# Optimization experiments

Measured on AMD Instinct MI355X. Metric: run time of the kernel, lower is better.

Reference implementation:

```python
import jax, jax.numpy as jnp
import numpy as np

N_NODES = 100000
N_EDGES = 1600000
DIM_IN, DIM_HID, DIM_OUT = 256, 128, 64


def _gcn_norm(edge_index, num_nodes):
    # PyG gcn_norm with add_self_loops=True, symmetric normalization.
    loop = jnp.arange(num_nodes, dtype=edge_index.dtype)
    row = jnp.concatenate([edge_index[0], loop])  # source
    col = jnp.concatenate([edge_index[1], loop])  # destination
    deg = jax.ops.segment_sum(jnp.ones_like(col, dtype=jnp.float32), col,
                              num_segments=num_nodes)
    dis = jnp.where(deg > 0, jax.lax.rsqrt(deg), 0.0)
    norm = dis[row] * dis[col]  # [E + N]
    return row, col, norm


def _gcn_conv(x, row, col, norm, W, b, num_nodes):
    h = x @ W                      # [N, d_out] linear first (d_out <= d_in typical)
    msg = h[row] * norm[:, None]   # gather + edge scaling, [E+N, d_out]
    out = jax.ops.segment_sum(msg, col, num_segments=num_nodes)  # scatter-add
    return out + b


def setup_inputs() -> dict:
    key = jax.random.key(0)
    k1, k2, k3, k4, k5 = jax.random.split(key, 5)
    x = jax.random.normal(k1, (N_NODES, DIM_IN), dtype=jnp.float32)
    edge_index = jax.random.randint(k2, (2, N_EDGES), 0, N_NODES, dtype=jnp.int32)
    s1 = 1.0 / np.sqrt(DIM_IN)
    s2 = 1.0 / np.sqrt(DIM_HID)
    W1 = jax.random.uniform(k3, (DIM_IN, DIM_HID), jnp.float32, -s1, s1)
    b1 = jnp.zeros((DIM_HID,), jnp.float32)
    W2 = jax.random.uniform(k4, (DIM_HID, DIM_OUT), jnp.float32, -s2, s2)
    b2 = jnp.zeros((DIM_OUT,), jnp.float32)
    return {"x": x, "edge_index": edge_index, "W1": W1, "b1": b1,
            "W2": W2, "b2": b2}


def reference(x, edge_index, W1, b1, W2, b2):
    n = x.shape[0]
    row, col, norm = _gcn_norm(edge_index, n)  # cached=True: shared by both layers
    h = _gcn_conv(x, row, col, norm, W1, b1, n)
    h = jax.nn.relu(h)
    h = _gcn_conv(h, row, col, norm, W2, b2, n)
    return jax.nn.log_softmax(h, axis=-1)
```

## Files before the change

### kernel.cpp

```cpp
#include <hip/hip_runtime.h>

#define N_NODES 100000
#define N_EDGES 1600000
#define DIN 256
#define DHID 128
#define DOUT 64

#define BSHIFT 9
#define NBUCKET 196
#define CHUNK 4096
#define NCHUNK ((N_EDGES + CHUNK - 1) / CHUNK)

typedef __attribute__((ext_vector_type(8))) short bf16x8;
typedef __attribute__((ext_vector_type(4))) float f32x4;
typedef __attribute__((ext_vector_type(2))) float f32x2;

static __device__ __forceinline__ ushort f2bf(float f) {
  union { float f; uint u; } a; a.f = f;
  uint u = a.u;
  uint r = u + 0x7fffu + ((u >> 16) & 1u);
  return (ushort)(r >> 16);
}


#if __has_builtin(__builtin_amdgcn_cvt_pk_f32_fp8) && __has_builtin(__builtin_amdgcn_cvt_pk_fp8_f32) && __has_builtin(__builtin_amdgcn_cvt_f32_fp8)
#define FP8_HW 1
#else
#define FP8_HW 0
#endif

static __device__ __forceinline__ uint f2fp8(float f) {
#if FP8_HW
  return (uint)(__builtin_amdgcn_cvt_pk_fp8_f32(f, f, 0, false) & 0xFF);
#else
  uint u = __float_as_uint(f);
  uint s = (u >> 24) & 0x80u;
  u &= 0x7FFFFFFFu;
  u += 0x7FFFFu + ((u >> 20) & 1u);
  int e = (int)(u >> 23) - 120;
  uint m = (u >> 20) & 7u;
  uint v = (e <= 0) ? 0u : ((e >= 15) ? 0x7Eu : (((uint)e << 3) | m));
  return s | v;
#endif
}

static __device__ __forceinline__ f32x2 fp8x2f(uint v) {
#if FP8_HW
  return __builtin_amdgcn_cvt_pk_f32_fp8(v, false);
#else
  uint lo = v & 0xFFu, hi = (v >> 8) & 0xFFu;
  uint mlo = lo & 0x7Fu, mhi = hi & 0x7Fu;
  uint blo = (mlo ? ((mlo << 4) + 0x3C00u) : 0u) | ((lo & 0x80u) << 8);
  uint bhi = (mhi ? ((mhi << 4) + 0x3C00u) : 0u) | ((hi & 0x80u) << 8);
  f32x2 r;
  r.x = __uint_as_float(blo << 16);
  r.y = __uint_as_float(bhi << 16);
  return r;
#endif
}


__global__ __launch_bounds__(256) void k_hist(const int* __restrict__ colp,
                                              int* __restrict__ cntmat) {
  __shared__ int h[NBUCKET];
  int c = blockIdx.x;
  for (int i = threadIdx.x; i < NBUCKET; i += 256) h[i] = 0;
  __syncthreads();
  int e0 = c * CHUNK, e1 = min(e0 + CHUNK, N_EDGES);
  for (int e = e0 + threadIdx.x; e < e1; e += 256)
    atomicAdd(&h[colp[e] >> BSHIFT], 1);
  __syncthreads();
  for (int i = threadIdx.x; i < NBUCKET; i += 256)
    cntmat[c * NBUCKET + i] = h[i];
}


__global__ __launch_bounds__(256) void k_buckettot(const int* __restrict__ cntmat,
                                                   int* __restrict__ btot) {
  __shared__ int s[256];
  int b = blockIdx.x, t = threadIdx.x;
  int sum = 0;
  for (int c = t; c < NCHUNK; c += 256) sum += cntmat[c * NBUCKET + b];
  s[t] = sum;
  __syncthreads();
  for (int d = 128; d > 0; d >>= 1) {
    if (t < d) s[t] += s[t + d];
    __syncthreads();
  }
  if (t == 0) btot[b] = s[0];
}


__global__ void k_bucketscan(const int* __restrict__ btot, int* __restrict__ bbase) {
  __shared__ int s[256];
  int t = threadIdx.x;
  int v = (t < NBUCKET) ? btot[t] : 0;
  s[t] = v;
  __syncthreads();
  for (int d = 1; d < 256; d <<= 1) {
    int y = (t >= d) ? s[t - d] : 0;
    __syncthreads();
    s[t] += y;
    __syncthreads();
  }
  if (t < NBUCKET) bbase[t] = s[t] - v;
  if (t == 0) bbase[NBUCKET] = N_EDGES;
}


__global__ __launch_bounds__(256) void k_chunkpfx(const int* __restrict__ cntmat,
                                                  const int* __restrict__ bbase,
                                                  int* __restrict__ basemat) {
  int wid = blockIdx.x * 4 + (threadIdx.x >> 6);
  int lane = threadIdx.x & 63;
  if (wid >= NBUCKET) return;
  int carry = bbase[wid];
  const int NT = (NCHUNK + 63) / 64;
  for (int tt = 0; tt < NT; tt++) {
    int c = tt * 64 + lane;
    int v = (c < NCHUNK) ? cntmat[c * NBUCKET + wid] : 0;
    int incl = v;
#pragma unroll
    for (int d = 1; d < 64; d <<= 1) {
      int y = __shfl_up(incl, d, 64);
      if (lane >= d) incl += y;
    }
    if (c < NCHUNK) basemat[c * NBUCKET + wid] = carry + incl - v;
    carry += __shfl(incl, 63, 64);
  }
}


__global__ __launch_bounds__(256) void k_binscatter(const int* __restrict__ rowp,
                                                    const int* __restrict__ colp,
                                                    const int* __restrict__ basemat,
                                                    uint* __restrict__ packed) {
  __shared__ int lcur[NBUCKET];
  int c = blockIdx.x;
  for (int i = threadIdx.x; i < NBUCKET; i += 256)
    lcur[i] = basemat[c * NBUCKET + i];
  __syncthreads();
  int e0 = c * CHUNK, e1 = min(e0 + CHUNK, N_EDGES);
  for (int e = e0 + threadIdx.x; e < e1; e += 256) {
    int dst = colp[e], src = rowp[e];
    int pos = atomicAdd(&lcur[dst >> BSHIFT], 1);
    packed[pos] = (uint)src | ((uint)(dst & 511) << 17);
  }
}


__global__ __launch_bounds__(256) void k_count512(const uint* __restrict__ packed,
                                                  const int* __restrict__ bbase,
                                                  int* __restrict__ off,
                                                  float* __restrict__ dis) {
  __shared__ int cnt512[512];
  __shared__ int off512[512];
  __shared__ int s[256];
  int b = blockIdx.x, t = threadIdx.x;
  int node0 = b << BSHIFT;
  int nn = min(512, N_NODES - node0);
  for (int i = t; i < 512; i += 256) cnt512[i] = 0;
  __syncthreads();
  int r0 = bbase[b], r1 = bbase[b + 1];
  for (int r = r0 + t; r < r1; r += 256)
    atomicAdd(&cnt512[packed[r] >> 17], 1);
  __syncthreads();
  int c0 = cnt512[2 * t], c1 = cnt512[2 * t + 1];
  int ps = c0 + c1;
  s[t] = ps;
  __syncthreads();
  for (int d = 1; d < 256; d <<= 1) {
    int y = (t >= d) ? s[t - d] : 0;
    __syncthreads();
    s[t] += y;
    __syncthreads();
  }
  int ex = s[t] - ps;
  off512[2 * t] = ex;
  off512[2 * t + 1] = ex + c0;
  __syncthreads();
  for (int i = t; i < nn; i += 256) {
    off[node0 + i] = r0 + off512[i];
    dis[node0 + i] = rsqrtf((float)cnt512[i] + 1.0f);
  }
  if (b == NBUCKET - 1 && t == 0) off[N_NODES] = N_EDGES;
}


__global__ __launch_bounds__(256) void k_place(const uint* __restrict__ packed,
                                               const int* __restrict__ bbase,
                                               const int* __restrict__ off,
                                               const float* __restrict__ dis,
                                               uint* __restrict__ ep) {
  __shared__ int cur512[512];
  __shared__ int offl[512];
  int b = blockIdx.x, t = threadIdx.x;
  int node0 = b << BSHIFT;
  int nn = min(512, N_NODES - node0);
  for (int i = t; i < 512; i += 256) cur512[i] = 0;
  for (int i = t; i < nn; i += 256) offl[i] = off[node0 + i];
  __syncthreads();
  int r0 = bbase[b], r1 = bbase[b + 1];
  for (int r = r0 + t; r < r1; r += 256) {
    uint sd = packed[r];
    int d0 = sd >> 17;
    uint src = sd & 0x1FFFFu;
    float w = dis[src];
    uint w15 = min((uint)(w * 32768.0f + 0.5f), 32767u);
    int pos = offl[d0] + atomicAdd(&cur512[d0], 1);
    ep[pos] = src | (w15 << 17);
  }
}


__global__ void k_packW(const float* __restrict__ W1, ushort* __restrict__ Wp1,
                        const float* __restrict__ W2, ushort* __restrict__ Wp2) {
  int t = blockIdx.x * 256 + threadIdx.x;
  if (t < 8 * 8 * 64) {
    int l = t & 63, ks = (t >> 6) & 7, nt = t >> 9;
    int k0 = ks * 32 + (l >> 4) * 8;
    int n = nt * 16 + (l & 15);
    ushort* dst = Wp1 + (size_t)t * 8;
#pragma unroll
    for (int i = 0; i < 8; i++) dst[i] = f2bf(W1[(k0 + i) * DHID + n]);
  } else if (t < 8 * 8 * 64 + 4 * 4 * 64) {
    int t2 = t - 8 * 8 * 64;
    int l = t2 & 63, ks = (t2 >> 6) & 3, nt = t2 >> 8;
    int k0 = ks * 32 + (l >> 4) * 8;
    int n = nt * 16 + (l & 15);
    ushort* dst = Wp2 + (size_t)t2 * 8;
#pragma unroll
    for (int i = 0; i < 8; i++) dst[i] = f2bf(W2[(k0 + i) * DOUT + n]);
  }
}


__global__ __launch_bounds__(256) void k_gemm1(const float* __restrict__ x,
                                               const ushort* __restrict__ Wp,
                                               uchar* __restrict__ h1) {
  __shared__ uchar cs[4][16][144];
  int w = threadIdx.x >> 6, l = threadIdx.x & 63;
  int row0 = blockIdx.x * 64 + w * 16;
  bool valid = (row0 < N_NODES);
  if (valid) {
    f32x4 acc[8];
#pragma unroll
    for (int i = 0; i < 8; i++) acc[i] = (f32x4)(0.f);
    int arow = row0 + (l & 15);
    const float4* xg = (const float4*)(x + (size_t)arow * DIN) + (l >> 4) * 2;
    const bf16x8* wp = (const bf16x8*)Wp;
    float4 a[16];
#pragma unroll
    for (int ks = 0; ks < 8; ks++) {
      a[2 * ks]     = xg[ks * 8];
      a[2 * ks + 1] = xg[ks * 8 + 1];
    }
#pragma unroll
    for (int ks = 0; ks < 8; ks++) {
      float4 a0 = a[2 * ks];
      float4 a1 = a[2 * ks + 1];
      bf16x8 af;
      af[0] = (short)f2bf(a0.x); af[1] = (short)f2bf(a0.y);
      af[2] = (short)f2bf(a0.z); af[3] = (short)f2bf(a0.w);
      af[4] = (short)f2bf(a1.x); af[5] = (short)f2bf(a1.y);
      af[6] = (short)f2bf(a1.z); af[7] = (short)f2bf(a1.w);
#pragma unroll
      for (int nt = 0; nt < 8; nt++) {
        bf16x8 bf = wp[(nt * 8 + ks) * 64 + l];
        acc[nt] = __builtin_amdgcn_mfma_f32_16x16x32_bf16(af, bf, acc[nt], 0, 0, 0);
      }
    }
#pragma unroll
    for (int nt = 0; nt < 8; nt++)
#pragma unroll
      for (int r = 0; r < 4; r++)
        cs[w][(l >> 4) * 4 + r][nt * 16 + (l & 15)] = (uchar)f2fp8(acc[nt][r]);
  }
  __syncthreads();
  if (valid) {
    const uint4* s4 = (const uint4*)&cs[w][l >> 2][(l & 3) * 32];
    uint4* dst = (uint4*)(h1 + (size_t)(row0 + (l >> 2)) * DHID + (l & 3) * 32);
    dst[0] = s4[0]; dst[1] = s4[1];
  }
}


#define AGG1_BATCH4(eX, pfx)                                                    \
  {                                                                             \
    uint p0 = ep[eX], p1 = ep[eX + 1], p2 = ep[eX + 2], p3 = ep[eX + 3];        \
    ushort v0 = h1[(size_t)(p0 & 0x1FFFFu) * 64 + lane];                        \
    ushort v1 = h1[(size_t)(p1 & 0x1FFFFu) * 64 + lane];                        \
    ushort v2 = h1[(size_t)(p2 & 0x1FFFFu) * 64 + lane];                        \
    ushort v3 = h1[(size_t)(p3 & 0x1FFFFu) * 64 + lane];                        \
    f32x2 f0 = fp8x2f(v0), f1 = fp8x2f(v1), f2 = fp8x2f(v2), f3 = fp8x2f(v3);   \
    float w0 = (float)(p0 >> 17) * 0x1p-15f;                                    \
    float w1 = (float)(p1 >> 17) * 0x1p-15f;                                    \
    float w2 = (float)(p2 >> 17) * 0x1p-15f;                                    \
    float w3 = (float)(p3 >> 17) * 0x1p-15f;                                    \
    ax##pfx = fmaf(f0.x, w0, ax##pfx); ay##pfx = fmaf(f0.y, w0, ay##pfx);       \
    ax##pfx = fmaf(f1.x, w1, ax##pfx); ay##pfx = fmaf(f1.y, w1, ay##pfx);       \
    ax##pfx = fmaf(f2.x, w2, ax##pfx); ay##pfx = fmaf(f2.y, w2, ay##pfx);       \
    ax##pfx = fmaf(f3.x, w3, ax##pfx); ay##pfx = fmaf(f3.y, w3, ay##pfx);       \
  }

#define AGG1_TAIL(eX, eX1, pfx)                                                 \
  for (; eX < eX1; eX++) {                                                      \
    uint p = ep[eX];                                                            \
    f32x2 f0 = fp8x2f(h1[(size_t)(p & 0x1FFFFu) * 64 + lane]);                  \
    float w0 = (float)(p >> 17) * 0x1p-15f;                                     \
    ax##pfx = fmaf(f0.x, w0, ax##pfx); ay##pfx = fmaf(f0.y, w0, ay##pfx);       \
  }

__global__ __launch_bounds__(256) void k_agg1g2(const ushort* __restrict__ h1,
                                                const int* __restrict__ off,
                                                const uint* __restrict__ ep,
                                                const float* __restrict__ dis,
                                                const float* __restrict__ b1,
                                                const ushort* __restrict__ Wp2,
                                                uchar* __restrict__ h2) {
  __shared__ ushort as[16][136];
  int w = threadIdx.x >> 6, lane = threadIdx.x & 63;
  int nb0 = blockIdx.x * 16;
  float2 bb = ((const float2*)b1)[lane];
  int widA = nb0 + w * 4;
  float dA = dis[widA], dB = dis[widA + 1], dC = dis[widA + 2], dD = dis[widA + 3];
  f32x2 hvA = fp8x2f(h1[(size_t)widA * 64 + lane]);
  f32x2 hvB = fp8x2f(h1[(size_t)(widA + 1) * 64 + lane]);
  f32x2 hvC = fp8x2f(h1[(size_t)(widA + 2) * 64 + lane]);
  f32x2 hvD = fp8x2f(h1[(size_t)(widA + 3) * 64 + lane]);
  float axA = hvA.x * dA, ayA = hvA.y * dA;
  float axB = hvB.x * dB, ayB = hvB.y * dB;
  float axC = hvC.x * dC, ayC = hvC.y * dC;
  float axD = hvD.x * dD, ayD = hvD.y * dD;
  int eA  = __builtin_amdgcn_readfirstlane(off[widA]);
  int eA1 = __builtin_amdgcn_readfirstlane(off[widA + 1]);
  int eB  = eA1;
  int eB1 = __builtin_amdgcn_readfirstlane(off[widA + 2]);
  int eC  = eB1;
  int eC1 = __builtin_amdgcn_readfirstlane(off[widA + 3]);
  int eD  = eC1;
  int eD1 = __builtin_amdgcn_readfirstlane(off[widA + 4]);
  while (eA + 4 <= eA1 && eB + 4 <= eB1 && eC + 4 <= eC1 && eD + 4 <= eD1) {
    AGG1_BATCH4(eA, A)
    AGG1_BATCH4(eB, B)
    AGG1_BATCH4(eC, C)
    AGG1_BATCH4(eD, D)
    eA += 4; eB += 4; eC += 4; eD += 4;
  }
  while (eA + 4 <= eA1 && eB + 4 <= eB1) {
    AGG1_BATCH4(eA, A)
    AGG1_BATCH4(eB, B)
    eA += 4; eB += 4;
  }
  while (eC + 4 <= eC1 && eD + 4 <= eD1) {
    AGG1_BATCH4(eC, C)
    AGG1_BATCH4(eD, D)
    eC += 4; eD += 4;
  }
  for (; eA + 4 <= eA1; eA += 4) AGG1_BATCH4(eA, A)
  for (; eB + 4 <= eB1; eB += 4) AGG1_BATCH4(eB, B)
  for (; eC + 4 <= eC1; eC += 4) AGG1_BATCH4(eC, C)
  for (; eD + 4 <= eD1; eD += 4) AGG1_BATCH4(eD, D)
  AGG1_TAIL(eA, eA1, A)
  AGG1_TAIL(eB, eB1, B)
  AGG1_TAIL(eC, eC1, C)
  AGG1_TAIL(eD, eD1, D)
  {
    float rx, ry;
    rx = fmaxf(fmaf(dA, axA, bb.x), 0.f); ry = fmaxf(fmaf(dA, ayA, bb.y), 0.f);
    ((uint*)&as[w * 4 + 0][0])[lane] = (uint)f2bf(rx) | ((uint)f2bf(ry) << 16);
    rx = fmaxf(fmaf(dB, axB, bb.x), 0.f); ry = fmaxf(fmaf(dB, ayB, bb.y), 0.f);
    ((uint*)&as[w * 4 + 1][0])[lane] = (uint)f2bf(rx) | ((uint)f2bf(ry) << 16);
    rx = fmaxf(fmaf(dC, axC, bb.x), 0.f); ry = fmaxf(fmaf(dC, ayC, bb.y), 0.f);
    ((uint*)&as[w * 4 + 2][0])[lane] = (uint)f2bf(rx) | ((uint)f2bf(ry) << 16);
    rx = fmaxf(fmaf(dD, axD, bb.x), 0.f); ry = fmaxf(fmaf(dD, ayD, bb.y), 0.f);
    ((uint*)&as[w * 4 + 3][0])[lane] = (uint)f2bf(rx) | ((uint)f2bf(ry) << 16);
  }
  __syncthreads();
  f32x4 acc = (f32x4)(0.f);
  const bf16x8* wp = (const bf16x8*)Wp2;
#pragma unroll
  for (int ks = 0; ks < 4; ks++) {
    bf16x8 af = *(const bf16x8*)&as[lane & 15][ks * 32 + (lane >> 4) * 8];
    bf16x8 bf = wp[(w * 4 + ks) * 64 + lane];
    acc = __builtin_amdgcn_mfma_f32_16x16x32_bf16(af, bf, acc, 0, 0, 0);
  }
#pragma unroll
  for (int r = 0; r < 4; r++) {
    int row = (lane >> 4) * 4 + r;
    h2[(size_t)(nb0 + row) * DOUT + w * 16 + (lane & 15)] = (uchar)f2fp8(acc[r]);
  }
}


#define AGG2_BATCH4(eX)                                                         \
  {                                                                             \
    uint p0 = ep[eX], p1 = ep[eX + 1], p2 = ep[eX + 2], p3 = ep[eX + 3];        \
    uint v0 = h2u[(size_t)(p0 & 0x1FFFFu) * 16 + q];                            \
    uint v1 = h2u[(size_t)(p1 & 0x1FFFFu) * 16 + q];                            \
    uint v2 = h2u[(size_t)(p2 & 0x1FFFFu) * 16 + q];                            \
    uint v3 = h2u[(size_t)(p3 & 0x1FFFFu) * 16 + q];                            \
    float w0 = (float)(p0 >> 17) * 0x1p-15f;                                    \
    float w1 = (float)(p1 >> 17) * 0x1p-15f;                                    \
    float w2 = (float)(p2 >> 17) * 0x1p-15f;                                    \
    float w3 = (float)(p3 >> 17) * 0x1p-15f;                                    \
    f32x2 l0 = fp8x2f(v0), h0 = fp8x2f(v0 >> 16);                               \
    f32x2 l1 = fp8x2f(v1), h1_ = fp8x2f(v1 >> 16);                              \
    f32x2 l2 = fp8x2f(v2), h2_ = fp8x2f(v2 >> 16);                              \
    f32x2 l3 = fp8x2f(v3), h3_ = fp8x2f(v3 >> 16);                              \
    a0 = fmaf(l0.x, w0, a0); a1 = fmaf(l0.y, w0, a1);                           \
    a2 = fmaf(h0.x, w0, a2); a3 = fmaf(h0.y, w0, a3);                           \
    a0 = fmaf(l1.x, w1, a0); a1 = fmaf(l1.y, w1, a1);                           \
    a2 = fmaf(h1_.x, w1, a2); a3 = fmaf(h1_.y, w1, a3);                         \
    a0 = fmaf(l2.x, w2, a0); a1 = fmaf(l2.y, w2, a1);                           \
    a2 = fmaf(h2_.x, w2, a2); a3 = fmaf(h2_.y, w2, a3);                         \
    a0 = fmaf(l3.x, w3, a0); a1 = fmaf(l3.y, w3, a1);                           \
    a2 = fmaf(h3_.x, w3, a2); a3 = fmaf(h3_.y, w3, a3);                         \
  }

__global__ __launch_bounds__(256) void k_agg2(const uint* __restrict__ h2u,
                                              const int* __restrict__ off,
                                              const uint* __restrict__ ep,
                                              const float* __restrict__ dis,
                                              const float* __restrict__ b2,
                                              float* __restrict__ out) {
  int gw   = (blockIdx.x * 256 + threadIdx.x) >> 6;
  int lane = threadIdx.x & 63;
  int g = lane >> 4;
  int q = lane & 15;
  int wid = gw * 4 + g;
  if (wid >= N_NODES) return;
  float d = dis[wid];
  uint sv = h2u[(size_t)wid * 16 + q];
  f32x2 slo = fp8x2f(sv), shi = fp8x2f(sv >> 16);
  float a0 = slo.x * d, a1 = slo.y * d, a2 = shi.x * d, a3 = shi.y * d;
  int o0 = off[wid], o1 = off[wid + 1];
  int e = o0;
  for (; e + 4 <= o1; e += 4) AGG2_BATCH4(e)
  for (; e < o1; e++) {
    uint p = ep[e];
    uint v = h2u[(size_t)(p & 0x1FFFFu) * 16 + q];
    float w = (float)(p >> 17) * 0x1p-15f;
    f32x2 lo = fp8x2f(v), hi = fp8x2f(v >> 16);
    a0 = fmaf(lo.x, w, a0); a1 = fmaf(lo.y, w, a1);
    a2 = fmaf(hi.x, w, a2); a3 = fmaf(hi.y, w, a3);
  }
  float4 bbv = ((const float4*)b2)[q];
  float v0 = fmaf(d, a0, bbv.x);
  float v1 = fmaf(d, a1, bbv.y);
  float v2 = fmaf(d, a2, bbv.z);
  float v3 = fmaf(d, a3, bbv.w);
  float m = fmaxf(fmaxf(v0, v1), fmaxf(v2, v3));
#pragma unroll
  for (int sft = 8; sft >= 1; sft >>= 1) m = fmaxf(m, __shfl_xor(m, sft, 64));
  float sum = expf(v0 - m) + expf(v1 - m) + expf(v2 - m) + expf(v3 - m);
#pragma unroll
  for (int sft = 8; sft >= 1; sft >>= 1) sum += __shfl_xor(sum, sft, 64);
  float ls = m + logf(sum);
  float4 o;
  o.x = v0 - ls; o.y = v1 - ls; o.z = v2 - ls; o.w = v3 - ls;
  ((float4*)out)[(size_t)wid * 16 + q] = o;
}


extern "C" void kernel_launch(void* const* d_in, const int* in_sizes, int n_in,
                              void* d_out, int out_size, void* d_ws, size_t ws_size,
                              hipStream_t stream) {
  const float* x  = (const float*)d_in[0];
  const int*   ei = (const int*)d_in[1];
  const float* W1 = (const float*)d_in[2];
  const float* b1 = (const float*)d_in[3];
  const float* W2 = (const float*)d_in[4];
  const float* b2 = (const float*)d_in[5];
  float* out = (float*)d_out;
  const int* rowp = ei;
  const int* colp = ei + N_EDGES;

  char* p = (char*)d_ws;
  size_t o = 0;
  auto alloc = [&](size_t bytes) -> void* {
    void* r = p + o;
    o = (o + bytes + 255) & ~(size_t)255;
    return r;
  };
  int*    off    = (int*)alloc((size_t)(N_NODES + 1) * 4);
  float*  dis    = (float*)alloc((size_t)N_NODES * 4);
  int*    cntmat = (int*)alloc((size_t)NCHUNK * NBUCKET * 4);
  int*    basemat= (int*)alloc((size_t)NCHUNK * NBUCKET * 4);
  int*    btot   = (int*)alloc((size_t)NBUCKET * 4);
  int*    bbase  = (int*)alloc((size_t)(NBUCKET + 1) * 4);
  uint*   packed = (uint*)alloc((size_t)N_EDGES * 4);
  uint*   ep     = (uint*)alloc((size_t)N_EDGES * 4);
  ushort* Wp1    = (ushort*)alloc((size_t)8 * 8 * 64 * 8 * 2);
  ushort* Wp2    = (ushort*)alloc((size_t)4 * 4 * 64 * 8 * 2);
  uchar*  h1     = (uchar*)alloc((size_t)N_NODES * DHID);
  uchar*  h2     = (uchar*)alloc((size_t)N_NODES * DOUT);

  k_hist<<<NCHUNK, 256, 0, stream>>>(colp, cntmat);
  k_buckettot<<<NBUCKET, 256, 0, stream>>>(cntmat, btot);
  k_bucketscan<<<1, 256, 0, stream>>>(btot, bbase);
  k_chunkpfx<<<(NBUCKET + 3) / 4, 256, 0, stream>>>(cntmat, bbase, basemat);
  k_binscatter<<<NCHUNK, 256, 0, stream>>>(rowp, colp, basemat, packed);
  k_count512<<<NBUCKET, 256, 0, stream>>>(packed, bbase, off, dis);
  k_place<<<NBUCKET, 256, 0, stream>>>(packed, bbase, off, dis, ep);
  k_packW<<<20, 256, 0, stream>>>(W1, Wp1, W2, Wp2);
  k_gemm1<<<(N_NODES + 63) / 64, 256, 0, stream>>>(x, Wp1, h1);
  k_agg1g2<<<N_NODES / 16, 256, 0, stream>>>((const ushort*)h1, off, ep, dis, b1, Wp2, h2);
  k_agg2<<<N_NODES / 16, 256, 0, stream>>>((const uint*)h2, off, ep, dis, b2, out);
}
```

Before: 161.4 us.

## Merge bucket total and scan kernels; stage GEMM1 A tile in swizzled LDS

```diff
diff --git a/kernel.cpp b/kernel.cpp
--- a/kernel.cpp
+++ b/kernel.cpp
@@ -75,27 +75,16 @@
 }
 
 
-__global__ __launch_bounds__(256) void k_buckettot(const int* __restrict__ cntmat,
-                                                   int* __restrict__ btot) {
-  __shared__ int s[256];
-  int b = blockIdx.x, t = threadIdx.x;
-  int sum = 0;
-  for (int c = t; c < NCHUNK; c += 256) sum += cntmat[c * NBUCKET + b];
-  s[t] = sum;
-  __syncthreads();
-  for (int d = 128; d > 0; d >>= 1) {
-    if (t < d) s[t] += s[t + d];
-    __syncthreads();
-  }
-  if (t == 0) btot[b] = s[0];
-}
-
-
-__global__ void k_bucketscan(const int* __restrict__ btot, int* __restrict__ bbase) {
+__global__ __launch_bounds__(256) void k_bucket(const int* __restrict__ cntmat,
+                                                int* __restrict__ bbase) {
   __shared__ int s[256];
   int t = threadIdx.x;
-  int v = (t < NBUCKET) ? btot[t] : 0;
-  s[t] = v;
+  int sum = 0;
+  if (t < NBUCKET) {
+#pragma unroll 4
+    for (int c = 0; c < NCHUNK; c++) sum += cntmat[c * NBUCKET + t];
+  }
+  s[t] = sum;
   __syncthreads();
   for (int d = 1; d < 256; d <<= 1) {
     int y = (t >= d) ? s[t - d] : 0;
@@ -103,7 +92,7 @@
     s[t] += y;
     __syncthreads();
   }
-  if (t < NBUCKET) bbase[t] = s[t] - v;
+  if (t < NBUCKET) bbase[t] = s[t] - sum;
   if (t == 0) bbase[NBUCKET] = N_EDGES;
 }
 
@@ -238,32 +227,37 @@
 __global__ __launch_bounds__(256) void k_gemm1(const float* __restrict__ x,
                                                const ushort* __restrict__ Wp,
                                                uchar* __restrict__ h1) {
+  __shared__ ushort as[64 * 256];
   __shared__ uchar cs[4][16][144];
-  int w = threadIdx.x >> 6, l = threadIdx.x & 63;
-  int row0 = blockIdx.x * 64 + w * 16;
-  bool valid = (row0 < N_NODES);
+  int t = threadIdx.x;
+  int w = t >> 6, l = t & 63;
+  int row0 = blockIdx.x * 64;
+  const float4* xg4 = (const float4*)x;
+#pragma unroll
+  for (int it = 0; it < 16; it++) {
+    int f = it * 256 + t;
+    int r = f >> 6, c4 = f & 63;
+    int gr = row0 + r;
+    float4 v = make_float4(0.f, 0.f, 0.f, 0.f);
+    if (gr < N_NODES) v = xg4[(size_t)gr * 64 + c4];
+    ushort4 bv;
+    bv.x = f2bf(v.x); bv.y = f2bf(v.y); bv.z = f2bf(v.z); bv.w = f2bf(v.w);
+    int j = c4 >> 1, half = c4 & 1;
+    int idx = r * 256 + ((j ^ (r & 7)) << 3) + half * 4;
+    *(ushort4*)&as[idx] = bv;
+  }
+  __syncthreads();
+  bool valid = (row0 + w * 16 < N_NODES);
   if (valid) {
     f32x4 acc[8];
 #pragma unroll
     for (int i = 0; i < 8; i++) acc[i] = (f32x4)(0.f);
-    int arow = row0 + (l & 15);
-    const float4* xg = (const float4*)(x + (size_t)arow * DIN) + (l >> 4) * 2;
     const bf16x8* wp = (const bf16x8*)Wp;
-    float4 a[16];
+    int r = w * 16 + (l & 15);
 #pragma unroll
     for (int ks = 0; ks < 8; ks++) {
-      a[2 * ks]     = xg[ks * 8];
-      a[2 * ks + 1] = xg[ks * 8 + 1];
-    }
-#pragma unroll
-    for (int ks = 0; ks < 8; ks++) {
-      float4 a0 = a[2 * ks];
-      float4 a1 = a[2 * ks + 1];
-      bf16x8 af;
-      af[0] = (short)f2bf(a0.x); af[1] = (short)f2bf(a0.y);
-      af[2] = (short)f2bf(a0.z); af[3] = (short)f2bf(a0.w);
-      af[4] = (short)f2bf(a1.x); af[5] = (short)f2bf(a1.y);
-      af[6] = (short)f2bf(a1.z); af[7] = (short)f2bf(a1.w);
+      int j = ks * 4 + (l >> 4);
+      bf16x8 af = *(const bf16x8*)&as[r * 256 + ((j ^ (r & 7)) << 3)];
 #pragma unroll
       for (int nt = 0; nt < 8; nt++) {
         bf16x8 bf = wp[(nt * 8 + ks) * 64 + l];
@@ -273,13 +267,13 @@
 #pragma unroll
     for (int nt = 0; nt < 8; nt++)
 #pragma unroll
-      for (int r = 0; r < 4; r++)
-        cs[w][(l >> 4) * 4 + r][nt * 16 + (l & 15)] = (uchar)f2fp8(acc[nt][r]);
+      for (int rr = 0; rr < 4; rr++)
+        cs[w][(l >> 4) * 4 + rr][nt * 16 + (l & 15)] = (uchar)f2fp8(acc[nt][rr]);
   }
   __syncthreads();
   if (valid) {
     const uint4* s4 = (const uint4*)&cs[w][l >> 2][(l & 3) * 32];
-    uint4* dst = (uint4*)(h1 + (size_t)(row0 + (l >> 2)) * DHID + (l & 3) * 32);
+    uint4* dst = (uint4*)(h1 + (size_t)(row0 + w * 16 + (l >> 2)) * DHID + (l & 3) * 32);
     dst[0] = s4[0]; dst[1] = s4[1];
   }
 }
@@ -487,7 +481,6 @@
   float*  dis    = (float*)alloc((size_t)N_NODES * 4);
   int*    cntmat = (int*)alloc((size_t)NCHUNK * NBUCKET * 4);
   int*    basemat= (int*)alloc((size_t)NCHUNK * NBUCKET * 4);
-  int*    btot   = (int*)alloc((size_t)NBUCKET * 4);
   int*    bbase  = (int*)alloc((size_t)(NBUCKET + 1) * 4);
   uint*   packed = (uint*)alloc((size_t)N_EDGES * 4);
   uint*   ep     = (uint*)alloc((size_t)N_EDGES * 4);
@@ -497,8 +490,7 @@
   uchar*  h2     = (uchar*)alloc((size_t)N_NODES * DOUT);
 
   k_hist<<<NCHUNK, 256, 0, stream>>>(colp, cntmat);
-  k_buckettot<<<NBUCKET, 256, 0, stream>>>(cntmat, btot);
-  k_bucketscan<<<1, 256, 0, stream>>>(btot, bbase);
+  k_bucket<<<1, 256, 0, stream>>>(cntmat, bbase);
   k_chunkpfx<<<(NBUCKET + 3) / 4, 256, 0, stream>>>(cntmat, bbase, basemat);
   k_binscatter<<<NCHUNK, 256, 0, stream>>>(rowp, colp, basemat, packed);
   k_count512<<<NBUCKET, 256, 0, stream>>>(packed, bbase, off, dis);
```

New measurement: 194.8 us. 1.21x slower.
